# Optimization experiments

Hardware: AMD Instinct MI355X
Metric: run time of the kernel (lower is better)

## Reference

```python
import jax, jax.numpy as jnp
import numpy as np

B, S, HID = 2, 2048, 2048
NH, G = 32, 4            # num_attn_heads, num_attn_groups
HD = HID // NH           # 64 head_dim
HKV = NH // G            # 8 query/key heads
THETA = 10000.0


def setup_inputs() -> dict:
    key = jax.random.key(0)
    k1, k2, k3, k4 = jax.random.split(key, 4)
    s = 0.02
    return {
        "hidden_states": jax.random.normal(k1, (B, S, HID), jnp.float32),
        "position_ids": jnp.broadcast_to(jnp.arange(S, dtype=jnp.int32)[None, :], (B, S)),
        "Wq": jax.random.normal(k2, (HID, HKV * HD), jnp.float32) * s,
        "Wk": jax.random.normal(k3, (HID, HKV * HD), jnp.float32) * s,
        "Wv": jax.random.normal(k4, (HID, NH * HD), jnp.float32) * s,
    }


def _rotate_half(x):
    x1, x2 = jnp.split(x, 2, axis=-1)
    return jnp.concatenate([-x2, x1], axis=-1)


def reference(hidden_states, position_ids, Wq, Wk, Wv):
    b, s, hid = hidden_states.shape
    # Q/K use HKV heads, V uses all NH heads
    Q = (hidden_states @ Wq).reshape(b, s, HKV, HD)
    K = (hidden_states @ Wk).reshape(b, s, HKV, HD)
    V = (hidden_states @ Wv).reshape(b, s, NH, HD)

    # RoPE (seq_len <= max_position_embeddings, no NTK rescale branch)
    inv_freq = 1.0 / (THETA ** (jnp.arange(0, HD, 2, dtype=jnp.float32) / HD))
    freqs = position_ids.astype(jnp.float32)[:, :, None] * inv_freq[None, None, :]  # [B,S,HD/2]
    emb = jnp.concatenate([freqs, freqs], axis=-1)                                   # [B,S,HD]
    cos = jnp.cos(emb)[:, :, None, :]  # unsqueeze head dim
    sin = jnp.sin(emb)[:, :, None, :]
    Q = Q * cos + _rotate_half(Q) * sin
    K = K * cos + _rotate_half(K) * sin

    # repeat_qk: [B,S,HKV,HD] -> [B,S,G*HKV,HD], head index = r*HKV + h
    def rep(x):
        return jnp.broadcast_to(x[:, :, None, :, :], (b, s, G, HKV, HD)).reshape(b, s, NH, HD)
    Q = rep(Q)
    K = rep(K)

    # causal SDPA
    scale = 1.0 / np.sqrt(HD).astype(np.float32)
    scores = jnp.einsum('bqhd,bkhd->bhqk', Q, K) * scale          # [B,NH,S,S]
    causal = jnp.tril(jnp.ones((s, s), dtype=bool))
    scores = jnp.where(causal[None, None, :, :], scores, jnp.float32(-1e9))
    attn = jax.nn.softmax(scores, axis=-1)
    out = jnp.einsum('bhqk,bkhd->bqhd', attn, V)                  # [B,S,NH,HD]
    return out.reshape(b, s, hid)
```

## Files before the change

### kernel.cpp

```cpp
#include <hip/hip_runtime.h>
#include <hip/hip_bf16.h>

typedef unsigned short u16;
typedef unsigned int   u32;
typedef __attribute__((ext_vector_type(8))) short bf16x8;
typedef __attribute__((ext_vector_type(4))) float f32x4;

#define B_   2
#define S_   2048
#define HID_ 2048
#define NH_  32
#define HKV_ 8
#define HD_  64
#define NQK  512
#define NTOT 3072
#define MROWS 4096

__device__ __forceinline__ u16 f2bf(float f) {
  u32 x = __float_as_uint(f);
  x += 0x7fffu + ((x >> 16) & 1u);
  return (u16)(x >> 16);
}
__device__ __forceinline__ float bf2f(u16 u) { return __uint_as_float(((u32)u) << 16); }
__device__ __forceinline__ u32 pack2bf(float a, float b) {
  return (u32)f2bf(a) | ((u32)f2bf(b) << 16);
}

__device__ __forceinline__ void gload16(const u16* g, u16* l) {
  __builtin_amdgcn_global_load_lds((const __attribute__((address_space(1))) void*)g,
                                   (__attribute__((address_space(3))) void*)l, 16, 0, 0);
}

__global__ __launch_bounds__(256) void cvtA_kernel(const float* __restrict__ A,
                                                   u16* __restrict__ Abf) {
  const int n4 = (MROWS * HID_) / 4;
  int i = blockIdx.x * blockDim.x + threadIdx.x;
  for (int idx = i; idx < n4; idx += gridDim.x * blockDim.x) {
    float4 v = ((const float4*)A)[idx];
    ushort4 o;
    o.x = f2bf(v.x); o.y = f2bf(v.y); o.z = f2bf(v.z); o.w = f2bf(v.w);
    ((ushort4*)Abf)[idx] = o;
  }
}

__global__ __launch_bounds__(256) void cvtW_kernel(const float* __restrict__ Wq,
                                                   const float* __restrict__ Wk,
                                                   const float* __restrict__ Wv,
                                                   u16* __restrict__ Wt) {
  int n0 = blockIdx.x * 32, k0 = blockIdx.y * 32;
  const float* src; int ld, nn;
  if (n0 < 512)       { src = Wq; nn = n0;        ld = 512;  }
  else if (n0 < 1024) { src = Wk; nn = n0 - 512;  ld = 512;  }
  else                { src = Wv; nn = n0 - 1024; ld = 2048; }
  __shared__ float tile[32][33];
  int tx = threadIdx.x, ty = threadIdx.y;
#pragma unroll
  for (int i = 0; i < 4; i++) {
    int kk = k0 + ty + i * 8;
    tile[ty + i * 8][tx] = src[(size_t)kk * ld + nn + tx];
  }
  __syncthreads();
#pragma unroll
  for (int i = 0; i < 4; i++) {
    int nrow = ty + i * 8;
    Wt[(size_t)(n0 + nrow) * HID_ + k0 + tx] = f2bf(tile[tx][nrow]);
  }
}

__global__ __launch_bounds__(256) void gemm_kernel(const u16* __restrict__ A,
                                                   const u16* __restrict__ Bt,
                                                   u16* __restrict__ C) {
  __shared__ u16 As[128 * 64];
  __shared__ u16 Bs[128 * 64];
  bf16x8* Asv = (bf16x8*)As;
  bf16x8* Bsv = (bf16x8*)Bs;
  int tid = threadIdx.x, l = tid & 63, wid = tid >> 6;
  int l15 = l & 15, lg = l >> 4;
  int bm = blockIdx.y * 128, bn = blockIdx.x * 128;
  int wr = (wid >> 1) * 64, wc = (wid & 1) * 64;
  f32x4 acc[4][4] = {};
  int r_[4], c_[4];
#pragma unroll
  for (int i = 0; i < 4; i++) {
    int slot = i * 256 + tid;
    int r = slot >> 3, sub = slot & 7;
    r_[i] = r;
    c_[i] = (sub ^ (r & 7)) << 3;
  }
  for (int kt = 0; kt < HID_ / 64; kt++) {
    int k0 = kt * 64;
    __syncthreads();
#pragma unroll
    for (int i = 0; i < 4; i++)
      gload16(A + (size_t)(bm + r_[i]) * HID_ + k0 + c_[i], (u16*)&Asv[i * 256 + wid * 64]);
#pragma unroll
    for (int i = 0; i < 4; i++)
      gload16(Bt + (size_t)(bn + r_[i]) * HID_ + k0 + c_[i], (u16*)&Bsv[i * 256 + wid * 64]);
    __syncthreads();
#pragma unroll
    for (int kc = 0; kc < 2; kc++) {
      bf16x8 af[4], bfr[4];
      int sub = kc * 4 + lg;
#pragma unroll
      for (int m = 0; m < 4; m++) {
        int row = wr + m * 16 + l15;
        af[m] = Asv[row * 8 + (sub ^ (row & 7))];
      }
#pragma unroll
      for (int n = 0; n < 4; n++) {
        int row = wc + n * 16 + l15;
        bfr[n] = Bsv[row * 8 + (sub ^ (row & 7))];
      }
#pragma unroll
      for (int m = 0; m < 4; m++)
#pragma unroll
        for (int n = 0; n < 4; n++)
          acc[m][n] = __builtin_amdgcn_mfma_f32_16x16x32_bf16(af[m], bfr[n], acc[m][n], 0, 0, 0);
    }
  }
#pragma unroll
  for (int m = 0; m < 4; m++)
#pragma unroll
    for (int n = 0; n < 4; n++) {
      int col  = bn + wc + n * 16 + l15;
      int rowb = bm + wr + m * 16 + lg * 4;
#pragma unroll
      for (int j = 0; j < 4; j++)
        C[(size_t)(rowb + j) * NTOT + col] = f2bf(acc[m][n][j]);
    }
}

__global__ __launch_bounds__(128) void rope_kernel(const u16* __restrict__ QKV,
                                                   const int* __restrict__ pos_ids,
                                                   u16* __restrict__ Qr,
                                                   u16* __restrict__ Kr) {
  int bs = blockIdx.x;
  int b = bs >> 11, s = bs & 2047;
  __shared__ float cs[32], sn[32];
  int t = threadIdx.x;
  if (t < 32) {
    float inv = expf(-((float)(2 * t) / 64.0f) * logf(10000.0f));
    float ang = (float)pos_ids[bs] * inv;
    cs[t] = cosf(ang);
    sn[t] = sinf(ang);
  }
  __syncthreads();
  const u16* row = QKV + (size_t)bs * NTOT;
#pragma unroll
  for (int i = 0; i < 4; i++) {
    int e = t + i * 128;
    int h = e >> 6, d = e & 63, j = d & 31;
    int ep = (d < 32) ? e + 32 : e - 32;
    size_t dst = (((size_t)(b * HKV_ + h) * S_ + s) * HD_) + d;
    float xq = bf2f(row[e]),        xq2 = bf2f(row[ep]);
    float xk = bf2f(row[NQK + e]),  xk2 = bf2f(row[NQK + ep]);
    float qv = (d < 32) ? xq * cs[j] - xq2 * sn[j] : xq * cs[j] + xq2 * sn[j];
    float kv = (d < 32) ? xk * cs[j] - xk2 * sn[j] : xk * cs[j] + xk2 * sn[j];
    Qr[dst] = f2bf(qv * 0.125f);
    Kr[dst] = f2bf(kv);
  }
}

__global__ __launch_bounds__(256) void transV_kernel(const u16* __restrict__ QKV,
                                                     u16* __restrict__ Vt) {
  int st = blockIdx.x, h = blockIdx.y, b = blockIdx.z;
  __shared__ u16 tile[64][65];
  int t = threadIdx.x;
#pragma unroll
  for (int i = 0; i < 16; i++) {
    int idx = t + i * 256;
    int r = idx >> 6, d = idx & 63;
    tile[r][d] = QKV[(size_t)(b * S_ + st * 64 + r) * NTOT + 1024 + h * 64 + d];
  }
  __syncthreads();
#pragma unroll
  for (int i = 0; i < 16; i++) {
    int idx = t + i * 256;
    int d = idx >> 6, ss = idx & 63;
    Vt[((size_t)(b * NH_ + h) * HD_ + d) * S_ + st * 64 + ss] = tile[ss][d];
  }
}

__global__ __launch_bounds__(64, 1) void attn_kernel(const u16* __restrict__ Qr,
                                                     const u16* __restrict__ Kr,
                                                     const u16* __restrict__ Vt,
                                                     float* __restrict__ Out) {
  int bx = blockIdx.x;
  int hk = blockIdx.y, b = blockIdx.z;
  int qt = ((hk >> 2) & 1) ? (63 - bx) : bx;
  int l = threadIdx.x, l15 = l & 15, g = l >> 4;
  int qb = qt * 32;

  __shared__ u16 Plds[32 * 64];

  const u16* Qbase = Qr + (size_t)(b * HKV_ + hk) * S_ * HD_;
  const u16* Kbase = Kr + (size_t)(b * HKV_ + hk) * S_ * HD_;
  const u16* Vb[4];
#pragma unroll
  for (int r = 0; r < 4; r++)
    Vb[r] = Vt + (size_t)(b * NH_ + r * 8 + hk) * HD_ * S_;

  bf16x8 bq[2][2];
#pragma unroll
  for (int nq = 0; nq < 2; nq++)
#pragma unroll
    for (int kc = 0; kc < 2; kc++)
      bq[nq][kc] = *(const bf16x8*)(Qbase + (size_t)(qb + nq * 16 + l15) * HD_ + kc * 32 + g * 8);

  f32x4 O[4][2][4] = {};
  float mS[2] = {-1e30f, -1e30f}, lS[2] = {0.f, 0.f};

  int ntiles = (qb + 95) >> 6;

  bf16x8 ka[2][4];
#pragma unroll
  for (int kc = 0; kc < 2; kc++)
#pragma unroll
    for (int mk = 0; mk < 4; mk++)
      ka[kc][mk] = *(const bf16x8*)(Kbase + (size_t)(mk * 16 + l15) * HD_ + kc * 32 + g * 8);

  for (int kt = 0; kt < ntiles; kt++) {
    f32x4 sacc[4][2] = {};
#pragma unroll
    for (int kc = 0; kc < 2; kc++)
#pragma unroll
      for (int mk = 0; mk < 4; mk++)
#pragma unroll
        for (int nq = 0; nq < 2; nq++)
          sacc[mk][nq] = __builtin_amdgcn_mfma_f32_16x16x32_bf16(ka[kc][mk], bq[nq][kc], sacc[mk][nq], 0, 0, 0);
    int ktn = (kt + 1 < ntiles) ? kt + 1 : kt;
    bf16x8 kan[2][4];
#pragma unroll
    for (int kc = 0; kc < 2; kc++)
#pragma unroll
      for (int mk = 0; mk < 4; mk++)
        kan[kc][mk] = *(const bf16x8*)(Kbase + (size_t)(ktn * 64 + mk * 16 + l15) * HD_ + kc * 32 + g * 8);
    float tmax[2] = {-1e30f, -1e30f};
#pragma unroll
    for (int mk = 0; mk < 4; mk++)
#pragma unroll
      for (int nq = 0; nq < 2; nq++)
#pragma unroll
        for (int j = 0; j < 4; j++) {
          int key = kt * 64 + mk * 16 + g * 4 + j;
          int q   = qb + nq * 16 + l15;
          float s = (key <= q) ? sacc[mk][nq][j] : -1e30f;
          sacc[mk][nq][j] = s;
          tmax[nq] = fmaxf(tmax[nq], s);
        }
#pragma unroll
    for (int nq = 0; nq < 2; nq++) {
      tmax[nq] = fmaxf(tmax[nq], __shfl_xor(tmax[nq], 16));
      tmax[nq] = fmaxf(tmax[nq], __shfl_xor(tmax[nq], 32));
    }
    bool need = (tmax[0] > mS[0] + 8.0f) || (tmax[1] > mS[1] + 8.0f);
    if (__any(need)) {
      float alpha[2];
#pragma unroll
      for (int nq = 0; nq < 2; nq++) {
        float mnew = fmaxf(mS[nq], tmax[nq]);
        alpha[nq] = __expf(mS[nq] - mnew);
        mS[nq] = mnew;
        lS[nq] *= alpha[nq];
      }
#pragma unroll
      for (int m = 0; m < 2; m++)
#pragma unroll
        for (int j = 0; j < 4; j++) {
          float a = __shfl(alpha[m], g * 4 + j);
#pragma unroll
          for (int r = 0; r < 4; r++)
#pragma unroll
            for (int nd = 0; nd < 4; nd++)
              O[r][m][nd][j] *= a;
        }
    }
    float tsum[2] = {0.f, 0.f};
    u32 upk[2][4][2];
#pragma unroll
    for (int nq = 0; nq < 2; nq++)
#pragma unroll
      for (int mk = 0; mk < 4; mk++) {
        float p0 = __expf(sacc[mk][nq][0] - mS[nq]);
        float p1 = __expf(sacc[mk][nq][1] - mS[nq]);
        float p2 = __expf(sacc[mk][nq][2] - mS[nq]);
        float p3 = __expf(sacc[mk][nq][3] - mS[nq]);
        tsum[nq] += (p0 + p1) + (p2 + p3);
        upk[nq][mk][0] = pack2bf(p0, p1);
        upk[nq][mk][1] = pack2bf(p2, p3);
      }
#pragma unroll
    for (int nq = 0; nq < 2; nq++) {
      tsum[nq] += __shfl_xor(tsum[nq], 16);
      tsum[nq] += __shfl_xor(tsum[nq], 32);
      lS[nq] += tsum[nq];
    }
#pragma unroll
    for (int nq = 0; nq < 2; nq++)
#pragma unroll
      for (int mk = 0; mk < 4; mk++) {
        int ql  = nq * 16 + l15;
        int sub = mk * 2 + (g >> 1);
        int byteoff = ql * 128 + ((sub ^ (ql & 7)) * 16) + (g & 1) * 8;
        *(uint2*)((char*)Plds + byteoff) = make_uint2(upk[nq][mk][0], upk[nq][mk][1]);
      }
#pragma unroll
    for (int kc = 0; kc < 2; kc++) {
      bf16x8 pa[2];
#pragma unroll
      for (int m = 0; m < 2; m++) {
        int ql  = m * 16 + l15;
        int sub = kc * 4 + g;
        pa[m] = *(bf16x8*)((char*)Plds + ql * 128 + ((sub ^ (ql & 7)) * 16));
      }
#pragma unroll
      for (int r = 0; r < 4; r++) {
        bf16x8 vb[4];
#pragma unroll
        for (int nd = 0; nd < 4; nd++) {
          int d = nd * 16 + l15;
          vb[nd] = *(const bf16x8*)(Vb[r] + (size_t)d * S_ + kt * 64 + kc * 32 + g * 8);
        }
#pragma unroll
        for (int m = 0; m < 2; m++)
#pragma unroll
          for (int nd = 0; nd < 4; nd++)
            O[r][m][nd] = __builtin_amdgcn_mfma_f32_16x16x32_bf16(pa[m], vb[nd], O[r][m][nd], 0, 0, 0);
      }
    }
#pragma unroll
    for (int kc = 0; kc < 2; kc++)
#pragma unroll
      for (int mk = 0; mk < 4; mk++)
        ka[kc][mk] = kan[kc][mk];
  }
  float linv[2];
#pragma unroll
  for (int m = 0; m < 2; m++) linv[m] = 1.0f / lS[m];
#pragma unroll
  for (int m = 0; m < 2; m++)
#pragma unroll
    for (int j = 0; j < 4; j++) {
      float li = __shfl(linv[m], g * 4 + j);
      int q = qb + m * 16 + g * 4 + j;
#pragma unroll
      for (int r = 0; r < 4; r++)
#pragma unroll
        for (int nd = 0; nd < 4; nd++) {
          int d = nd * 16 + l15;
          Out[(size_t)(b * S_ + q) * HID_ + (r * 8 + hk) * 64 + d] = O[r][m][nd][j] * li;
        }
    }
}

extern "C" void kernel_launch(void* const* d_in, const int* in_sizes, int n_in,
                              void* d_out, int out_size, void* d_ws, size_t ws_size,
                              hipStream_t stream) {
  const float* hs  = (const float*)d_in[0];
  const int*   pos = (const int*)d_in[1];
  const float* Wq  = (const float*)d_in[2];
  const float* Wk  = (const float*)d_in[3];
  const float* Wv  = (const float*)d_in[4];
  float* out = (float*)d_out;
  char* ws = (char*)d_ws;
  u16* Abf = (u16*)(ws + 0);
  u16* Wt  = (u16*)(ws + 16777216);
  u16* QKV = (u16*)(ws + 29360128);
  u16* Qr  = (u16*)(ws + 54525952);
  u16* Kr  = (u16*)(ws + 58720256);
  u16* Vt  = (u16*)(ws + 62914560);

  cvtA_kernel<<<dim3(2048), dim3(256), 0, stream>>>(hs, Abf);
  cvtW_kernel<<<dim3(96, 64), dim3(32, 8), 0, stream>>>(Wq, Wk, Wv, Wt);
  gemm_kernel<<<dim3(24, 32), dim3(256), 0, stream>>>(Abf, Wt, QKV);
  rope_kernel<<<dim3(4096), dim3(128), 0, stream>>>(QKV, pos, Qr, Kr);
  transV_kernel<<<dim3(32, 32, 2), dim3(256), 0, stream>>>(QKV, Vt);
  attn_kernel<<<dim3(64, 8, 2), dim3(64), 0, stream>>>(Qr, Kr, Vt, out);
}
```

Before: 286.5 us.

## Halve attention query tile to 16 rows and vectorize RoPE loads/stores

The attention kernel now processes 16 query rows per single-wave block instead of 32. That doubles the grid to 2048 blocks and raises launch bounds to allow two waves per SIMD, aiming for better occupancy and load balance across the GPU. In exchange, each K/V tile is re-read by twice as many blocks, and each block does less MFMA work per global load. Separately, the RoPE kernel now has each thread load its element and rotation partner as 8-wide bf16 vectors and write one 16-byte vector, replacing scalar loads and stores.

Measured after the change: 330.9 us. 1.16x slower.

```diff
diff --git a/kernel.cpp b/kernel.cpp
--- a/kernel.cpp
+++ b/kernel.cpp
@@ -146,19 +146,23 @@
   }
   __syncthreads();
   const u16* row = QKV + (size_t)bs * NTOT;
-#pragma unroll
-  for (int i = 0; i < 4; i++) {
-    int e = t + i * 128;
-    int h = e >> 6, d = e & 63, j = d & 31;
-    int ep = (d < 32) ? e + 32 : e - 32;
-    size_t dst = (((size_t)(b * HKV_ + h) * S_ + s) * HD_) + d;
-    float xq = bf2f(row[e]),        xq2 = bf2f(row[ep]);
-    float xk = bf2f(row[NQK + e]),  xk2 = bf2f(row[NQK + ep]);
-    float qv = (d < 32) ? xq * cs[j] - xq2 * sn[j] : xq * cs[j] + xq2 * sn[j];
-    float kv = (d < 32) ? xk * cs[j] - xk2 * sn[j] : xk * cs[j] + xk2 * sn[j];
-    Qr[dst] = f2bf(qv * 0.125f);
-    Kr[dst] = f2bf(kv);
-  }
+  int part = t >> 6;
+  int g2 = t & 63;
+  int h = g2 >> 3, seg = (g2 >> 2) & 1, d0 = (g2 & 3) * 8;
+  const u16* src = row + part * NQK + h * 64;
+  bf16x8 v = *(const bf16x8*)(src + seg * 32 + d0);
+  bf16x8 p = *(const bf16x8*)(src + (1 - seg) * 32 + d0);
+  float scale = part ? 1.0f : 0.125f;
+  u16 ov[8];
+#pragma unroll
+  for (int i = 0; i < 8; i++) {
+    int j = d0 + i;
+    float a = bf2f((u16)v[i]), q = bf2f((u16)p[i]);
+    float r = seg ? (a * cs[j] + q * sn[j]) : (a * cs[j] - q * sn[j]);
+    ov[i] = f2bf(r * scale);
+  }
+  u16* dst = (part ? Kr : Qr) + (((size_t)(b * HKV_ + h) * S_ + s) * HD_) + seg * 32 + d0;
+  *(bf16x8*)dst = *(bf16x8*)ov;
 }
 
 __global__ __launch_bounds__(256) void transV_kernel(const u16* __restrict__ QKV,
@@ -181,17 +185,17 @@
   }
 }
 
-__global__ __launch_bounds__(64, 1) void attn_kernel(const u16* __restrict__ Qr,
+__global__ __launch_bounds__(64, 2) void attn_kernel(const u16* __restrict__ Qr,
                                                      const u16* __restrict__ Kr,
                                                      const u16* __restrict__ Vt,
                                                      float* __restrict__ Out) {
   int bx = blockIdx.x;
   int hk = blockIdx.y, b = blockIdx.z;
-  int qt = ((hk >> 2) & 1) ? (63 - bx) : bx;
+  int qt = ((hk >> 2) & 1) ? (127 - bx) : bx;
   int l = threadIdx.x, l15 = l & 15, g = l >> 4;
-  int qb = qt * 32;
-
-  __shared__ u16 Plds[32 * 64];
+  int qb = qt * 16;
+
+  __shared__ u16 Plds[16 * 64];
 
   const u16* Qbase = Qr + (size_t)(b * HKV_ + hk) * S_ * HD_;
   const u16* Kbase = Kr + (size_t)(b * HKV_ + hk) * S_ * HD_;
@@ -200,17 +204,15 @@
   for (int r = 0; r < 4; r++)
     Vb[r] = Vt + (size_t)(b * NH_ + r * 8 + hk) * HD_ * S_;
 
-  bf16x8 bq[2][2];
-#pragma unroll
-  for (int nq = 0; nq < 2; nq++)
-#pragma unroll
-    for (int kc = 0; kc < 2; kc++)
-      bq[nq][kc] = *(const bf16x8*)(Qbase + (size_t)(qb + nq * 16 + l15) * HD_ + kc * 32 + g * 8);
-
-  f32x4 O[4][2][4] = {};
-  float mS[2] = {-1e30f, -1e30f}, lS[2] = {0.f, 0.f};
-
-  int ntiles = (qb + 95) >> 6;
+  bf16x8 bq[2];
+#pragma unroll
+  for (int kc = 0; kc < 2; kc++)
+    bq[kc] = *(const bf16x8*)(Qbase + (size_t)(qb + l15) * HD_ + kc * 32 + g * 8);
+
+  f32x4 O[4][4] = {};
+  float mS = -1e30f, lS = 0.f;
+
+  int ntiles = (qb + 79) >> 6;
 
   bf16x8 ka[2][4];
 #pragma unroll
@@ -220,14 +222,12 @@
       ka[kc][mk] = *(const bf16x8*)(Kbase + (size_t)(mk * 16 + l15) * HD_ + kc * 32 + g * 8);
 
   for (int kt = 0; kt < ntiles; kt++) {
-    f32x4 sacc[4][2] = {};
+    f32x4 sacc[4] = {};
 #pragma unroll
     for (int kc = 0; kc < 2; kc++)
 #pragma unroll
       for (int mk = 0; mk < 4; mk++)
-#pragma unroll
-        for (int nq = 0; nq < 2; nq++)
-          sacc[mk][nq] = __builtin_amdgcn_mfma_f32_16x16x32_bf16(ka[kc][mk], bq[nq][kc], sacc[mk][nq], 0, 0, 0);
+        sacc[mk] = __builtin_amdgcn_mfma_f32_16x16x32_bf16(ka[kc][mk], bq[kc], sacc[mk], 0, 0, 0);
     int ktn = (kt + 1 < ntiles) ? kt + 1 : kt;
     bf16x8 kan[2][4];
 #pragma unroll
@@ -235,84 +235,59 @@
 #pragma unroll
       for (int mk = 0; mk < 4; mk++)
         kan[kc][mk] = *(const bf16x8*)(Kbase + (size_t)(ktn * 64 + mk * 16 + l15) * HD_ + kc * 32 + g * 8);
-    float tmax[2] = {-1e30f, -1e30f};
+    float tmax = -1e30f;
+    int q = qb + l15;
 #pragma unroll
     for (int mk = 0; mk < 4; mk++)
 #pragma unroll
-      for (int nq = 0; nq < 2; nq++)
-#pragma unroll
-        for (int j = 0; j < 4; j++) {
-          int key = kt * 64 + mk * 16 + g * 4 + j;
-          int q   = qb + nq * 16 + l15;
-          float s = (key <= q) ? sacc[mk][nq][j] : -1e30f;
-          sacc[mk][nq][j] = s;
-          tmax[nq] = fmaxf(tmax[nq], s);
-        }
-#pragma unroll
-    for (int nq = 0; nq < 2; nq++) {
-      tmax[nq] = fmaxf(tmax[nq], __shfl_xor(tmax[nq], 16));
-      tmax[nq] = fmaxf(tmax[nq], __shfl_xor(tmax[nq], 32));
-    }
-    bool need = (tmax[0] > mS[0] + 8.0f) || (tmax[1] > mS[1] + 8.0f);
-    if (__any(need)) {
-      float alpha[2];
-#pragma unroll
-      for (int nq = 0; nq < 2; nq++) {
-        float mnew = fmaxf(mS[nq], tmax[nq]);
-        alpha[nq] = __expf(mS[nq] - mnew);
-        mS[nq] = mnew;
-        lS[nq] *= alpha[nq];
-      }
-#pragma unroll
-      for (int m = 0; m < 2; m++)
-#pragma unroll
-        for (int j = 0; j < 4; j++) {
-          float a = __shfl(alpha[m], g * 4 + j);
-#pragma unroll
-          for (int r = 0; r < 4; r++)
-#pragma unroll
-            for (int nd = 0; nd < 4; nd++)
-              O[r][m][nd][j] *= a;
-        }
-    }
-    float tsum[2] = {0.f, 0.f};
-    u32 upk[2][4][2];
-#pragma unroll
-    for (int nq = 0; nq < 2; nq++)
-#pragma unroll
-      for (int mk = 0; mk < 4; mk++) {
-        float p0 = __expf(sacc[mk][nq][0] - mS[nq]);
-        float p1 = __expf(sacc[mk][nq][1] - mS[nq]);
-        float p2 = __expf(sacc[mk][nq][2] - mS[nq]);
-        float p3 = __expf(sacc[mk][nq][3] - mS[nq]);
-        tsum[nq] += (p0 + p1) + (p2 + p3);
-        upk[nq][mk][0] = pack2bf(p0, p1);
-        upk[nq][mk][1] = pack2bf(p2, p3);
-      }
-#pragma unroll
-    for (int nq = 0; nq < 2; nq++) {
-      tsum[nq] += __shfl_xor(tsum[nq], 16);
-      tsum[nq] += __shfl_xor(tsum[nq], 32);
-      lS[nq] += tsum[nq];
-    }
-#pragma unroll
-    for (int nq = 0; nq < 2; nq++)
-#pragma unroll
-      for (int mk = 0; mk < 4; mk++) {
-        int ql  = nq * 16 + l15;
-        int sub = mk * 2 + (g >> 1);
-        int byteoff = ql * 128 + ((sub ^ (ql & 7)) * 16) + (g & 1) * 8;
-        *(uint2*)((char*)Plds + byteoff) = make_uint2(upk[nq][mk][0], upk[nq][mk][1]);
-      }
+      for (int j = 0; j < 4; j++) {
+        int key = kt * 64 + mk * 16 + g * 4 + j;
+        float s = (key <= q) ? sacc[mk][j] : -1e30f;
+        sacc[mk][j] = s;
+        tmax = fmaxf(tmax, s);
+      }
+    tmax = fmaxf(tmax, __shfl_xor(tmax, 16));
+    tmax = fmaxf(tmax, __shfl_xor(tmax, 32));
+    if (__any(tmax > mS + 8.0f)) {
+      float mnew = fmaxf(mS, tmax);
+      float alpha = __expf(mS - mnew);
+      mS = mnew;
+      lS *= alpha;
+#pragma unroll
+      for (int j = 0; j < 4; j++) {
+        float a = __shfl(alpha, g * 4 + j);
+#pragma unroll
+        for (int r = 0; r < 4; r++)
+#pragma unroll
+          for (int nd = 0; nd < 4; nd++)
+            O[r][nd][j] *= a;
+      }
+    }
+    float tsum = 0.f;
+    u32 upk[4][2];
+#pragma unroll
+    for (int mk = 0; mk < 4; mk++) {
+      float p0 = __expf(sacc[mk][0] - mS);
+      float p1 = __expf(sacc[mk][1] - mS);
+      float p2 = __expf(sacc[mk][2] - mS);
+      float p3 = __expf(sacc[mk][3] - mS);
+      tsum += (p0 + p1) + (p2 + p3);
+      upk[mk][0] = pack2bf(p0, p1);
+      upk[mk][1] = pack2bf(p2, p3);
+    }
+    tsum += __shfl_xor(tsum, 16);
+    tsum += __shfl_xor(tsum, 32);
+    lS += tsum;
+#pragma unroll
+    for (int mk = 0; mk < 4; mk++) {
+      int sub = mk * 2 + (g >> 1);
+      int byteoff = l15 * 128 + ((sub ^ (l15 & 7)) * 16) + (g & 1) * 8;
+      *(uint2*)((char*)Plds + byteoff) = make_uint2(upk[mk][0], upk[mk][1]);
+    }
 #pragma unroll
     for (int kc = 0; kc < 2; kc++) {
-      bf16x8 pa[2];
-#pragma unroll
-      for (int m = 0; m < 2; m++) {
-        int ql  = m * 16 + l15;
-        int sub = kc * 4 + g;
-        pa[m] = *(bf16x8*)((char*)Plds + ql * 128 + ((sub ^ (ql & 7)) * 16));
-      }
+      int sub = kc * 4 + g;
+      bf16x8 pa = *(bf16x8*)((char*)Plds + l15 * 128 + ((sub ^ (l15 & 7)) * 16));
 #pragma unroll
       for (int r = 0; r < 4; r++) {
         bf16x8 vb[4];
@@ -322,10 +297,8 @@
           vb[nd] = *(const bf16x8*)(Vb[r] + (size_t)d * S_ + kt * 64 + kc * 32 + g * 8);
         }
 #pragma unroll
-        for (int m = 0; m < 2; m++)
-#pragma unroll
-          for (int nd = 0; nd < 4; nd++)
-            O[r][m][nd] = __builtin_amdgcn_mfma_f32_16x16x32_bf16(pa[m], vb[nd], O[r][m][nd], 0, 0, 0);
+        for (int nd = 0; nd < 4; nd++)
+          O[r][nd] = __builtin_amdgcn_mfma_f32_16x16x32_bf16(pa, vb[nd], O[r][nd], 0, 0, 0);
       }
     }
 #pragma unroll
@@ -334,23 +307,19 @@
       for (int mk = 0; mk < 4; mk++)
         ka[kc][mk] = kan[kc][mk];
   }
-  float linv[2];
-#pragma unroll
-  for (int m = 0; m < 2; m++) linv[m] = 1.0f / lS[m];
-#pragma unroll
-  for (int m = 0; m < 2; m++)
-#pragma unroll
-    for (int j = 0; j < 4; j++) {
-      float li = __shfl(linv[m], g * 4 + j);
-      int q = qb + m * 16 + g * 4 + j;
-#pragma unroll
-      for (int r = 0; r < 4; r++)
-#pragma unroll
-        for (int nd = 0; nd < 4; nd++) {
-          int d = nd * 16 + l15;
-          Out[(size_t)(b * S_ + q) * HID_ + (r * 8 + hk) * 64 + d] = O[r][m][nd][j] * li;
-        }
-    }
+  float linv = 1.0f / lS;
+#pragma unroll
+  for (int j = 0; j < 4; j++) {
+    float li = __shfl(linv, g * 4 + j);
+    int q = qb + g * 4 + j;
+#pragma unroll
+    for (int r = 0; r < 4; r++)
+#pragma unroll
+      for (int nd = 0; nd < 4; nd++) {
+        int d = nd * 16 + l15;
+        Out[(size_t)(b * S_ + q) * HID_ + (r * 8 + hk) * 64 + d] = O[r][nd][j] * li;
+      }
+  }
 }
 
 extern "C" void kernel_launch(void* const* d_in, const int* in_sizes, int n_in,
@@ -375,5 +344,5 @@
   gemm_kernel<<<dim3(24, 32), dim3(256), 0, stream>>>(Abf, Wt, QKV);
   rope_kernel<<<dim3(4096), dim3(128), 0, stream>>>(QKV, pos, Qr, Kr);
   transV_kernel<<<dim3(32, 32, 2), dim3(256), 0, stream>>>(QKV, Vt);
-  attn_kernel<<<dim3(64, 8, 2), dim3(64), 0, stream>>>(Qr, Kr, Vt, out);
-}
+  attn_kernel<<<dim3(128, 8, 2), dim3(64), 0, stream>>>(Qr, Kr, Vt, out);
+}
```
